# Kernel tuning notes

Hardware: AMD Instinct MI355X
Metric: run time of the kernel (lower is better)

Reference implementation:

```python
import jax, jax.numpy as jnp
import numpy as np

N = 100000   # nodes
E = 1600000  # edges
F = 13       # input features
H = 128      # hidden dim
G = 512      # graphs in batch
C = 10       # classes
EPS = 1e-5   # BatchNorm eps


def setup_inputs() -> dict:
    key = jax.random.key(0)
    ks = jax.random.split(key, 12)
    inp = {
        "x": jax.random.normal(ks[0], (N, F), dtype=jnp.float32),
        "edge_index": jax.random.randint(ks[1], (2, E), 0, N, dtype=jnp.int64),
        "batch": jnp.sort(jax.random.randint(ks[2], (N,), 0, G, dtype=jnp.int64)),
        "W1": jax.random.normal(ks[3], (F, H), dtype=jnp.float32) / np.sqrt(F),
        "b1": jnp.zeros((H,), jnp.float32),
        "g1": jnp.ones((H,), jnp.float32), "be1": jnp.zeros((H,), jnp.float32),
        "m1": jnp.zeros((H,), jnp.float32), "v1": jnp.ones((H,), jnp.float32),
        "W2": jax.random.normal(ks[4], (H, H), dtype=jnp.float32) / np.sqrt(H),
        "b2": jnp.zeros((H,), jnp.float32),
        "g2": jnp.ones((H,), jnp.float32), "be2": jnp.zeros((H,), jnp.float32),
        "m2": jnp.zeros((H,), jnp.float32), "v2": jnp.ones((H,), jnp.float32),
        "W3": jax.random.normal(ks[5], (H, H), dtype=jnp.float32) / np.sqrt(H),
        "b3": jnp.zeros((H,), jnp.float32),
        "g3": jnp.ones((H,), jnp.float32), "be3": jnp.zeros((H,), jnp.float32),
        "m3": jnp.zeros((H,), jnp.float32), "v3": jnp.ones((H,), jnp.float32),
        "Wc1": jax.random.normal(ks[6], (H, H // 2), dtype=jnp.float32) / np.sqrt(H),
        "bc1": jnp.zeros((H // 2,), jnp.float32),
        "Wc2": jax.random.normal(ks[7], (H // 2, C), dtype=jnp.float32) / np.sqrt(H // 2),
        "bc2": jnp.zeros((C,), jnp.float32),
    }
    return inp


def reference(x, edge_index, batch,
              W1, b1, g1, be1, m1, v1,
              W2, b2, g2, be2, m2, v2,
              W3, b3, g3, be3, m3, v3,
              Wc1, bc1, Wc2, bc2):
    src, dst = edge_index[0], edge_index[1]
    n = x.shape[0]
    # GCN symmetric norm with self-loops: deg = in-degree(A) + 1
    deg = jax.ops.segment_sum(jnp.ones(src.shape[0], x.dtype), dst, num_segments=n) + 1.0
    dis = jax.lax.rsqrt(deg)                    # D^{-1/2}
    enorm = dis[src] * dis[dst]                 # per-edge norm [E]
    snorm = dis * dis                           # self-loop norm [N]

    def gcn(h, W, b):
        h = h @ W                               # [N,H]
        msg = h[src] * enorm[:, None]           # gather + scale [E,H]
        agg = jax.ops.segment_sum(msg, dst, num_segments=n)  # scatter-add
        return agg + h * snorm[:, None] + b

    def bn(h, g, be, m, v):                     # eval-mode BatchNorm1d
        return (h - m) * jax.lax.rsqrt(v + EPS) * g + be

    h = jax.nn.relu(bn(gcn(x, W1, b1), g1, be1, m1, v1))
    h = jax.nn.relu(bn(gcn(h, W2, b2), g2, be2, m2, v2))
    h = jax.nn.relu(bn(gcn(h, W3, b3), g3, be3, m3, v3))
    # dropout is identity in eval mode

    # global mean pool over graphs
    sums = jax.ops.segment_sum(h, batch, num_segments=G)            # [G,H]
    cnts = jax.ops.segment_sum(jnp.ones(n, h.dtype), batch, num_segments=G)
    pooled = sums / jnp.maximum(cnts, 1.0)[:, None]

    hid = jax.nn.relu(pooled @ Wc1 + bc1)
    logits = hid @ Wc2 + bc2                                        # [G,C]
    return logits
```

## Files before the change

### kernel.cpp

```cpp
#include <hip/hip_runtime.h>
#include <hip/hip_bf16.h>

#define EPS 1e-5f

typedef unsigned short u16;
typedef unsigned int u32;
typedef __attribute__((ext_vector_type(8))) short bf16x8;
typedef __attribute__((ext_vector_type(4))) float f32x4;

__device__ __forceinline__ u32 f2bf(float f) {
  u32 u = __float_as_uint(f);
  return (u + 0x7FFFu + ((u >> 16) & 1u)) >> 16;
}
__device__ __forceinline__ u32 pack2bf(float lo, float hi) {
  return f2bf(lo) | (f2bf(hi) << 16);
}
__device__ __forceinline__ float4 bf4(uint2 u) {
  float4 r;
  r.x = __uint_as_float(u.x << 16);
  r.y = __uint_as_float(u.x & 0xFFFF0000u);
  r.z = __uint_as_float(u.y << 16);
  r.w = __uint_as_float(u.y & 0xFFFF0000u);
  return r;
}

__global__ void k_hist_rank(const int* __restrict__ dst, int* __restrict__ cnt,
                            int* __restrict__ rank, int E) {
  int i = blockIdx.x * blockDim.x + threadIdx.x;
  int i4 = i << 2;
  if (i4 + 3 < E) {
    int d0 = dst[i4], d1 = dst[i4 + 1], d2 = dst[i4 + 2], d3 = dst[i4 + 3];
    int r0 = atomicAdd(&cnt[d0], 1);
    int r1 = atomicAdd(&cnt[d1], 1);
    int r2 = atomicAdd(&cnt[d2], 1);
    int r3 = atomicAdd(&cnt[d3], 1);
    rank[i4] = r0; rank[i4 + 1] = r1; rank[i4 + 2] = r2; rank[i4 + 3] = r3;
  } else {
    for (int e = i4; e < E; ++e) rank[e] = atomicAdd(&cnt[dst[e]], 1);
  }
}

__global__ void k_dis(const int* __restrict__ cnt, float* __restrict__ dis, int N) {
  int i = blockIdx.x * blockDim.x + threadIdx.x;
  if (i < N) dis[i] = rsqrtf((float)cnt[i] + 1.0f);
}

__global__ void k_scan_block(const int* __restrict__ in, int* __restrict__ out,
                             int* __restrict__ bsum, int N) {
  __shared__ int tmp[256];
  int lid = threadIdx.x;
  int i = blockIdx.x * 256 + lid;
  int v = (i < N) ? in[i] : 0;
  tmp[lid] = v;
  __syncthreads();
  for (int off = 1; off < 256; off <<= 1) {
    int t = (lid >= off) ? tmp[lid - off] : 0;
    __syncthreads();
    tmp[lid] += t;
    __syncthreads();
  }
  if (i < N) out[i] = tmp[lid] - v;
  if (lid == 255) bsum[blockIdx.x] = tmp[255];
}

__global__ void k_scan_bsum(const int* __restrict__ bsum, int* __restrict__ bexc, int nb) {
  __shared__ int tmp[512];
  int lid = threadIdx.x;
  int v = (lid < nb) ? bsum[lid] : 0;
  tmp[lid] = v;
  __syncthreads();
  for (int off = 1; off < 512; off <<= 1) {
    int t = (lid >= off) ? tmp[lid - off] : 0;
    __syncthreads();
    tmp[lid] += t;
    __syncthreads();
  }
  if (lid < nb) bexc[lid] = tmp[lid] - v;
}

__global__ void k_add_back(int* __restrict__ offs, const int* __restrict__ bexc,
                           int N, int E) {
  int i = blockIdx.x * 256 + threadIdx.x;
  if (i < N) offs[i] += bexc[blockIdx.x];
  if (i == 0) offs[N] = E;
}

__global__ void k_fill_rank(const int* __restrict__ src, const int* __restrict__ dst,
                            const int* __restrict__ rank, const int* __restrict__ offs,
                            int* __restrict__ csr, int E) {
  int i = blockIdx.x * blockDim.x + threadIdx.x;
  int i4 = i << 2;
  if (i4 + 3 < E) {
    int s0 = src[i4], s1 = src[i4 + 1], s2 = src[i4 + 2], s3 = src[i4 + 3];
    int d0 = dst[i4], d1 = dst[i4 + 1], d2 = dst[i4 + 2], d3 = dst[i4 + 3];
    int r0 = rank[i4], r1 = rank[i4 + 1], r2 = rank[i4 + 2], r3 = rank[i4 + 3];
    int p0 = offs[d0] + r0;
    int p1 = offs[d1] + r1;
    int p2 = offs[d2] + r2;
    int p3 = offs[d3] + r3;
    csr[p0] = s0; csr[p1] = s1; csr[p2] = s2; csr[p3] = s3;
  } else {
    for (int e = i4; e < E; ++e) csr[offs[dst[e]] + rank[e]] = src[e];
  }
}

__global__ void k_prep_w(const float* __restrict__ W2, const float* __restrict__ W3,
                         const float* __restrict__ b2, const float* __restrict__ g2,
                         const float* __restrict__ be2, const float* __restrict__ m2,
                         const float* __restrict__ v2,
                         const float* __restrict__ b3, const float* __restrict__ g3,
                         const float* __restrict__ be3, const float* __restrict__ m3,
                         const float* __restrict__ v3,
                         u16* __restrict__ Wht2, u16* __restrict__ Wlt2,
                         u16* __restrict__ Wht3, u16* __restrict__ Wlt3,
                         float* __restrict__ sc2, float* __restrict__ tc2,
                         float* __restrict__ sc3, float* __restrict__ tc3) {
  int idx = blockIdx.x * 256 + threadIdx.x;
  int layer = idx >> 14;
  int e = idx & 16383;
  int c = e >> 7, k = e & 127;
  const float* W = layer ? W3 : W2;
  float w = W[k * 128 + c];
  u32 h = f2bf(w);
  float l = w - __uint_as_float(h << 16);
  u16* Wh = layer ? Wht3 : Wht2;
  u16* Wl = layer ? Wlt3 : Wlt2;
  Wh[e] = (u16)h;
  Wl[e] = (u16)f2bf(l);
  if (e < 128) {
    int ch = e;
    const float* gg = layer ? g3 : g2;  const float* vv = layer ? v3 : v2;
    const float* be = layer ? be3 : be2; const float* mm = layer ? m3 : m2;
    const float* bb = layer ? b3 : b2;
    float s = gg[ch] * rsqrtf(vv[ch] + EPS);
    (layer ? sc3 : sc2)[ch] = s;
    (layer ? tc3 : tc2)[ch] = be[ch] + (bb[ch] - mm[ch]) * s;
  }
}

__global__ void k_padx_scale(const float* __restrict__ x, const float* __restrict__ dis,
                             float* __restrict__ xs, int N) {
  int i = blockIdx.x * blockDim.x + threadIdx.x;
  if (i >= N * 16) return;
  int n = i >> 4, f = i & 15;
  xs[i] = (f < 13) ? x[n * 13 + f] * dis[n] : 0.0f;
}

__global__ __launch_bounds__(64) void k_agg16(
    const float* __restrict__ xs, const int* __restrict__ csr,
    const int* __restrict__ offs, const float* __restrict__ dis,
    float* __restrict__ out, int N) {
  int node = (blockIdx.x << 2) + (threadIdx.x >> 4);
  int f = threadIdx.x & 15;
  if (node >= N) return;
  float a0 = xs[(size_t)node * 16 + f];
  float a1 = 0.f, a2 = 0.f, a3 = 0.f;
  int beg = offs[node], end = offs[node + 1];
  int i = beg;
  for (; i + 4 <= end; i += 4) {
    int s0 = csr[i], s1 = csr[i + 1], s2 = csr[i + 2], s3 = csr[i + 3];
    a0 += xs[(size_t)s0 * 16 + f];
    a1 += xs[(size_t)s1 * 16 + f];
    a2 += xs[(size_t)s2 * 16 + f];
    a3 += xs[(size_t)s3 * 16 + f];
  }
  for (; i < end; ++i) a0 += xs[(size_t)csr[i] * 16 + f];
  out[(size_t)node * 16 + f] = dis[node] * ((a0 + a1) + (a2 + a3));
}

__global__ __launch_bounds__(256) void k_gemm1(
    const float* __restrict__ ax, const float* __restrict__ W1,
    const float* __restrict__ bb, const float* __restrict__ gg,
    const float* __restrict__ be, const float* __restrict__ mm,
    const float* __restrict__ vv, const float* __restrict__ dis,
    u32* __restrict__ outb, int N) {
  int idx = blockIdx.x * 256 + threadIdx.x;
  if (idx >= N * 64) return;
  int node = idx >> 6, cp = idx & 63;
  int c0 = cp * 2, c1 = c0 + 1;
  float s0 = gg[c0] * rsqrtf(vv[c0] + EPS);
  float t0 = be[c0] + (bb[c0] - mm[c0]) * s0;
  float s1 = gg[c1] * rsqrtf(vv[c1] + EPS);
  float t1 = be[c1] + (bb[c1] - mm[c1]) * s1;
  float acc0 = 0.f, acc1 = 0.f;
#pragma unroll
  for (int k = 0; k < 13; ++k) {
    float av = ax[(size_t)node * 16 + k];
    acc0 = fmaf(av, W1[k * 128 + c0], acc0);
    acc1 = fmaf(av, W1[k * 128 + c1], acc1);
  }
  float dn = dis[node];
  float o0 = dn * fmaxf(fmaf(acc0, s0, t0), 0.f);
  float o1 = dn * fmaxf(fmaf(acc1, s1, t1), 0.f);
  outb[(size_t)node * 64 + cp] = pack2bf(o0, o1);
}

__global__ __launch_bounds__(256) void k_agg128(
    const u16* __restrict__ hb, const int* __restrict__ csr,
    const int* __restrict__ offs, const float* __restrict__ dis,
    uint2* __restrict__ Ahp, uint2* __restrict__ Alp, int N) {
  int node = (blockIdx.x << 2) + (threadIdx.x >> 6);
  if (node >= N) return;
  const int lane = threadIdx.x & 63;
  const int half = lane >> 5;
  const int q = lane & 31;
  const uint2* __restrict__ h2p = (const uint2*)hb;
  float dn = dis[node];
  int beg = offs[node], end = offs[node + 1];

  float4 sv = bf4(h2p[(size_t)node * 32 + q]);
  float wsf = half ? 0.f : 1.f;
  float4 a0 = make_float4(sv.x * wsf, sv.y * wsf, sv.z * wsf, sv.w * wsf);
  float4 z = make_float4(0.f, 0.f, 0.f, 0.f);
  float4 a1 = z, a2 = z, a3 = z, a4 = z, a5 = z, a6 = z, a7 = z;

  int i = beg;
  for (; i + 16 <= end; i += 16) {
    int s0 = csr[i +  0 + half];
    int s1 = csr[i +  2 + half];
    int s2 = csr[i +  4 + half];
    int s3 = csr[i +  6 + half];
    int s4 = csr[i +  8 + half];
    int s5 = csr[i + 10 + half];
    int s6 = csr[i + 12 + half];
    int s7 = csr[i + 14 + half];
    uint2 u0 = h2p[(size_t)s0 * 32 + q];
    uint2 u1 = h2p[(size_t)s1 * 32 + q];
    uint2 u2 = h2p[(size_t)s2 * 32 + q];
    uint2 u3 = h2p[(size_t)s3 * 32 + q];
    uint2 u4 = h2p[(size_t)s4 * 32 + q];
    uint2 u5 = h2p[(size_t)s5 * 32 + q];
    uint2 u6 = h2p[(size_t)s6 * 32 + q];
    uint2 u7 = h2p[(size_t)s7 * 32 + q];
    float4 v0 = bf4(u0), v1 = bf4(u1), v2 = bf4(u2), v3 = bf4(u3);
    float4 v4 = bf4(u4), v5 = bf4(u5), v6 = bf4(u6), v7 = bf4(u7);
    a0.x += v0.x; a0.y += v0.y; a0.z += v0.z; a0.w += v0.w;
    a1.x += v1.x; a1.y += v1.y; a1.z += v1.z; a1.w += v1.w;
    a2.x += v2.x; a2.y += v2.y; a2.z += v2.z; a2.w += v2.w;
    a3.x += v3.x; a3.y += v3.y; a3.z += v3.z; a3.w += v3.w;
    a4.x += v4.x; a4.y += v4.y; a4.z += v4.z; a4.w += v4.w;
    a5.x += v5.x; a5.y += v5.y; a5.z += v5.z; a5.w += v5.w;
    a6.x += v6.x; a6.y += v6.y; a6.z += v6.z; a6.w += v6.w;
    a7.x += v7.x; a7.y += v7.y; a7.z += v7.z; a7.w += v7.w;
  }
  for (; i < end; i += 2) {
    int j = i + half;
    int jc = (j < end) ? j : (end - 1);
    int s = csr[jc];
    float wt = (j < end) ? 1.f : 0.f;
    float4 v = bf4(h2p[(size_t)s * 32 + q]);
    a0.x = fmaf(v.x, wt, a0.x); a0.y = fmaf(v.y, wt, a0.y);
    a0.z = fmaf(v.z, wt, a0.z); a0.w = fmaf(v.w, wt, a0.w);
  }

  float4 r;
  r.x = ((a0.x + a1.x) + (a2.x + a3.x)) + ((a4.x + a5.x) + (a6.x + a7.x));
  r.y = ((a0.y + a1.y) + (a2.y + a3.y)) + ((a4.y + a5.y) + (a6.y + a7.y));
  r.z = ((a0.z + a1.z) + (a2.z + a3.z)) + ((a4.z + a5.z) + (a6.z + a7.z));
  r.w = ((a0.w + a1.w) + (a2.w + a3.w)) + ((a4.w + a5.w) + (a6.w + a7.w));
  r.x += __shfl_xor(r.x, 32, 64);
  r.y += __shfl_xor(r.y, 32, 64);
  r.z += __shfl_xor(r.z, 32, 64);
  r.w += __shfl_xor(r.w, 32, 64);
  if (half == 0) {
    r.x *= dn; r.y *= dn; r.z *= dn; r.w *= dn;
    u32 hx = f2bf(r.x), hy = f2bf(r.y), hz = f2bf(r.z), hw = f2bf(r.w);
    uint2 ph = make_uint2(hx | (hy << 16), hz | (hw << 16));
    float lx = r.x - __uint_as_float(hx << 16);
    float ly = r.y - __uint_as_float(hy << 16);
    float lz = r.z - __uint_as_float(hz << 16);
    float lw = r.w - __uint_as_float(hw << 16);
    uint2 pl = make_uint2(pack2bf(lx, ly), pack2bf(lz, lw));
    Ahp[(size_t)node * 32 + q] = ph;
    Alp[(size_t)node * 32 + q] = pl;
  }
}

template <bool OB>
__global__ __launch_bounds__(256) void k_gemm_mfma(
    const u16* __restrict__ Ah, const u16* __restrict__ Al,
    const u16* __restrict__ Wht, const u16* __restrict__ Wlt,
    const float* __restrict__ sc, const float* __restrict__ tc,
    const float* __restrict__ dis,
    float* __restrict__ outf, u16* __restrict__ outb, int N) {
  const int lane = threadIdx.x & 63;
  const int wv = threadIdx.x >> 6;
  const int r0 = blockIdx.x * 128 + wv * 32;
  const int lr = lane & 15;
  const int kg = lane >> 4;

  bf16x8 ahf[2][4], alf[2][4];
#pragma unroll
  for (int rt = 0; rt < 2; ++rt) {
    int row = min(r0 + rt * 16 + lr, N - 1);
    const bf16x8* pAh = (const bf16x8*)(Ah + (size_t)row * 128 + kg * 8);
    const bf16x8* pAl = (const bf16x8*)(Al + (size_t)row * 128 + kg * 8);
#pragma unroll
    for (int ks = 0; ks < 4; ++ks) {
      ahf[rt][ks] = pAh[ks * 4];
      alf[rt][ks] = pAl[ks * 4];
    }
  }
  float dr[2][4];
  if (OB) {
#pragma unroll
    for (int rt = 0; rt < 2; ++rt)
#pragma unroll
      for (int j = 0; j < 4; ++j)
        dr[rt][j] = dis[min(r0 + rt * 16 + kg * 4 + j, N - 1)];
  }

#pragma unroll
  for (int ct = 0; ct < 8; ++ct) {
    int c = ct * 16 + lr;
    const bf16x8* pBh = (const bf16x8*)(Wht + (size_t)c * 128 + kg * 8);
    const bf16x8* pBl = (const bf16x8*)(Wlt + (size_t)c * 128 + kg * 8);
    bf16x8 bh[4], bl[4];
#pragma unroll
    for (int ks = 0; ks < 4; ++ks) { bh[ks] = pBh[ks * 4]; bl[ks] = pBl[ks * 4]; }
    float s = sc[c], t = tc[c];
#pragma unroll
    for (int rt = 0; rt < 2; ++rt) {
      f32x4 acc = {0.f, 0.f, 0.f, 0.f};
#pragma unroll
      for (int ks = 0; ks < 4; ++ks) {
        acc = __builtin_amdgcn_mfma_f32_16x16x32_bf16(ahf[rt][ks], bh[ks], acc, 0, 0, 0);
        acc = __builtin_amdgcn_mfma_f32_16x16x32_bf16(alf[rt][ks], bh[ks], acc, 0, 0, 0);
        acc = __builtin_amdgcn_mfma_f32_16x16x32_bf16(ahf[rt][ks], bl[ks], acc, 0, 0, 0);
      }
#pragma unroll
      for (int j = 0; j < 4; ++j) {
        int row = r0 + rt * 16 + kg * 4 + j;
        if (row < N) {
          float o = fmaxf(fmaf(acc[j], s, t), 0.f);
          if (OB) {
            outb[(size_t)row * 128 + c] = (u16)f2bf(o * dr[rt][j]);
          } else {
            outf[(size_t)row * 128 + c] = o;
          }
        }
      }
    }
  }
}

__global__ void k_cnt_batch(const int* __restrict__ batch, int* __restrict__ cnt,
                            int N, int G) {
  int g = blockIdx.x * blockDim.x + threadIdx.x;
  if (g >= G) return;
  int lo = 0, hi = N;
  while (lo < hi) { int m = (lo + hi) >> 1; if (batch[m] < g) lo = m + 1; else hi = m; }
  int lb = lo;
  lo = 0; hi = N;
  while (lo < hi) { int m = (lo + hi) >> 1; if (batch[m] <= g) lo = m + 1; else hi = m; }
  cnt[g] = lo - lb;
}

__global__ __launch_bounds__(128) void k_pool(
    const float* __restrict__ h, const int* __restrict__ batch,
    float* __restrict__ pooled, int N) {
  int f = threadIdx.x;
  int n0 = blockIdx.x * 128;
  int nEnd = min(n0 + 128, N);
  float acc = 0.f;
  int cur = -1;
  for (int nn = n0; nn < nEnd; ++nn) {
    int g = batch[nn];
    if (g != cur) {
      if (cur >= 0) atomicAdd(&pooled[cur * 128 + f], acc);
      cur = g;
      acc = 0.f;
    }
    acc += h[(size_t)nn * 128 + f];
  }
  if (cur >= 0) atomicAdd(&pooled[cur * 128 + f], acc);
}

__global__ __launch_bounds__(64) void k_cls(
    const float* __restrict__ pooled, const int* __restrict__ cnt,
    const float* __restrict__ Wc1, const float* __restrict__ bc1,
    const float* __restrict__ Wc2, const float* __restrict__ bc2,
    float* __restrict__ out, int G) {
  __shared__ float pm[128];
  __shared__ float hid[64];
  int g = blockIdx.x, t = threadIdx.x;
  float invc = 1.f / fmaxf((float)cnt[g], 1.f);
  pm[t]      = pooled[g * 128 + t] * invc;
  pm[t + 64] = pooled[g * 128 + 64 + t] * invc;
  __syncthreads();
  float a = bc1[t];
#pragma unroll 8
  for (int k = 0; k < 128; ++k) a = fmaf(pm[k], Wc1[k * 64 + t], a);
  hid[t] = fmaxf(a, 0.f);
  __syncthreads();
  if (t < 10) {
    float a2 = bc2[t];
#pragma unroll
    for (int j = 0; j < 64; ++j) a2 = fmaf(hid[j], Wc2[j * 10 + t], a2);
    out[g * 10 + t] = a2;
  }
}

extern "C" void kernel_launch(void* const* d_in, const int* in_sizes, int n_in,
                              void* d_out, int out_size, void* d_ws, size_t ws_size,
                              hipStream_t stream) {
  const float* x   = (const float*)d_in[0];
  const int*   ei  = (const int*)d_in[1];
  const int* batch = (const int*)d_in[2];
  const float* W1 = (const float*)d_in[3];
  const float* b1 = (const float*)d_in[4];
  const float* g1 = (const float*)d_in[5];
  const float* be1 = (const float*)d_in[6];
  const float* m1 = (const float*)d_in[7];
  const float* v1 = (const float*)d_in[8];
  const float* W2 = (const float*)d_in[9];
  const float* b2 = (const float*)d_in[10];
  const float* g2 = (const float*)d_in[11];
  const float* be2 = (const float*)d_in[12];
  const float* m2 = (const float*)d_in[13];
  const float* v2 = (const float*)d_in[14];
  const float* W3 = (const float*)d_in[15];
  const float* b3 = (const float*)d_in[16];
  const float* g3 = (const float*)d_in[17];
  const float* be3 = (const float*)d_in[18];
  const float* m3 = (const float*)d_in[19];
  const float* v3 = (const float*)d_in[20];
  const float* Wc1 = (const float*)d_in[21];
  const float* bc1 = (const float*)d_in[22];
  const float* Wc2 = (const float*)d_in[23];
  const float* bc2 = (const float*)d_in[24];

  const int N = in_sizes[0] / 13;
  const int E = in_sizes[1] / 2;
  const int G = out_size / 10;
  const int* src = ei;
  const int* dst = ei + E;

  char* ws = (char*)d_ws;
  size_t off = 0;
  auto alloc = [&](size_t bytes) {
    char* p = ws + off;
    off = (off + bytes + 255) & ~(size_t)255;
    return p;
  };
  int*   deg    = (int*)  alloc((size_t)N * 4);
  float* dis    = (float*)alloc((size_t)N * 4);
  int*   offs   = (int*)  alloc((size_t)(N + 1) * 4);
  const int nb  = (N + 255) / 256;
  int*   bsum   = (int*)  alloc((size_t)nb * 4);
  int*   bexc   = (int*)  alloc((size_t)nb * 4);
  int*   rank   = (int*)  alloc((size_t)E * 4);
  int*   csr    = (int*)  alloc((size_t)E * 4);
  u16*   hbf    = (u16*)  alloc((size_t)N * 128 * 2);
  u16*   Ahp    = (u16*)  alloc((size_t)N * 128 * 2);
  u16*   Alp    = (u16*)  alloc((size_t)N * 128 * 2);
  float* bufF   = (float*)alloc((size_t)N * 128 * 4);
  u16*   Wht2   = (u16*)  alloc(16384 * 2);
  u16*   Wlt2   = (u16*)  alloc(16384 * 2);
  u16*   Wht3   = (u16*)  alloc(16384 * 2);
  u16*   Wlt3   = (u16*)  alloc(16384 * 2);
  float* sc2    = (float*)alloc(128 * 4);
  float* tc2    = (float*)alloc(128 * 4);
  float* sc3    = (float*)alloc(128 * 4);
  float* tc3    = (float*)alloc(128 * 4);
  float* pooled = (float*)alloc((size_t)G * 128 * 4);
  int*   cntg   = (int*)  alloc((size_t)G * 4);
  float* xs = bufF;
  float* ax = (float*)Ahp;

  hipMemsetAsync(deg, 0, (size_t)N * 4, stream);
  hipMemsetAsync(pooled, 0, (size_t)G * 128 * 4, stream);

  k_prep_w<<<128, 256, 0, stream>>>(W2, W3, b2, g2, be2, m2, v2, b3, g3, be3, m3, v3,
                                    Wht2, Wlt2, Wht3, Wlt3, sc2, tc2, sc3, tc3);

  const int nE4 = (E + 3) / 4;
  k_hist_rank<<<(nE4 + 255) / 256, 256, 0, stream>>>(dst, deg, rank, E);
  k_dis<<<(N + 255) / 256, 256, 0, stream>>>(deg, dis, N);
  k_scan_block<<<nb, 256, 0, stream>>>(deg, offs, bsum, N);
  k_scan_bsum<<<1, 512, 0, stream>>>(bsum, bexc, nb);
  k_add_back<<<nb, 256, 0, stream>>>(offs, bexc, N, E);
  k_fill_rank<<<(nE4 + 255) / 256, 256, 0, stream>>>(src, dst, rank, offs, csr, E);

  k_padx_scale<<<(N * 16 + 255) / 256, 256, 0, stream>>>(x, dis, xs, N);
  k_agg16<<<(N + 3) / 4, 64, 0, stream>>>(xs, csr, offs, dis, ax, N);
  k_gemm1<<<(N * 64 + 255) / 256, 256, 0, stream>>>(ax, W1, b1, g1, be1, m1, v1, dis,
                                                    (u32*)hbf, N);

  const int gemmGrid = (N + 127) / 128;
  k_agg128<<<(N + 3) / 4, 256, 0, stream>>>(hbf, csr, offs, dis,
                                            (uint2*)Ahp, (uint2*)Alp, N);
  k_gemm_mfma<true><<<gemmGrid, 256, 0, stream>>>(Ahp, Alp, Wht2, Wlt2, sc2, tc2, dis,
                                                  nullptr, hbf, N);
  k_agg128<<<(N + 3) / 4, 256, 0, stream>>>(hbf, csr, offs, dis,
                                            (uint2*)Ahp, (uint2*)Alp, N);
  k_gemm_mfma<false><<<gemmGrid, 256, 0, stream>>>(Ahp, Alp, Wht3, Wlt3, sc3, tc3, dis,
                                                   bufF, nullptr, N);

  k_cnt_batch<<<(G + 255) / 256, 256, 0, stream>>>(batch, cntg, N, G);
  k_pool<<<(N + 127) / 128, 128, 0, stream>>>(bufF, batch, pooled, N);
  k_cls<<<G, 64, 0, stream>>>(pooled, cntg, Wc1, bc1, Wc2, bc2, (float*)d_out, G);
}
```

Before: 640.4 us.

## Pad CSR rows to multiples of four with a zero dummy node, widen agg loads

```diff
diff --git a/kernel.cpp b/kernel.cpp
--- a/kernel.cpp
+++ b/kernel.cpp
@@ -15,13 +15,10 @@
 __device__ __forceinline__ u32 pack2bf(float lo, float hi) {
   return f2bf(lo) | (f2bf(hi) << 16);
 }
-__device__ __forceinline__ float4 bf4(uint2 u) {
-  float4 r;
-  r.x = __uint_as_float(u.x << 16);
-  r.y = __uint_as_float(u.x & 0xFFFF0000u);
-  r.z = __uint_as_float(u.y << 16);
-  r.w = __uint_as_float(u.y & 0xFFFF0000u);
-  return r;
+
+__device__ __forceinline__ void dacc(float2& a, u32 u) {
+  a.x += __uint_as_float(u << 16);
+  a.y += __uint_as_float(u & 0xFFFF0000u);
 }
 
 __global__ void k_hist_rank(const int* __restrict__ dst, int* __restrict__ cnt,
@@ -40,9 +37,14 @@
   }
 }
 
-__global__ void k_dis(const int* __restrict__ cnt, float* __restrict__ dis, int N) {
+__global__ void k_dis_pdeg(const int* __restrict__ cnt, float* __restrict__ dis,
+                           int* __restrict__ pdeg, int N) {
   int i = blockIdx.x * blockDim.x + threadIdx.x;
-  if (i < N) dis[i] = rsqrtf((float)cnt[i] + 1.0f);
+  if (i < N) {
+    int d = cnt[i];
+    dis[i] = rsqrtf((float)d + 1.0f);
+    pdeg[i] = (d + 3) & ~3;
+  }
 }
 
 __global__ void k_scan_block(const int* __restrict__ in, int* __restrict__ out,
@@ -79,10 +81,10 @@
 }
 
 __global__ void k_add_back(int* __restrict__ offs, const int* __restrict__ bexc,
-                           int N, int E) {
+                           const int* __restrict__ bsum, int N, int nb) {
   int i = blockIdx.x * 256 + threadIdx.x;
   if (i < N) offs[i] += bexc[blockIdx.x];
-  if (i == 0) offs[N] = E;
+  if (i == 0) offs[N] = bexc[nb - 1] + bsum[nb - 1];
 }
 
 __global__ void k_fill_rank(const int* __restrict__ src, const int* __restrict__ dst,
@@ -94,14 +96,21 @@
     int s0 = src[i4], s1 = src[i4 + 1], s2 = src[i4 + 2], s3 = src[i4 + 3];
     int d0 = dst[i4], d1 = dst[i4 + 1], d2 = dst[i4 + 2], d3 = dst[i4 + 3];
     int r0 = rank[i4], r1 = rank[i4 + 1], r2 = rank[i4 + 2], r3 = rank[i4 + 3];
-    int p0 = offs[d0] + r0;
-    int p1 = offs[d1] + r1;
-    int p2 = offs[d2] + r2;
-    int p3 = offs[d3] + r3;
-    csr[p0] = s0; csr[p1] = s1; csr[p2] = s2; csr[p3] = s3;
+    csr[offs[d0] + r0] = s0;
+    csr[offs[d1] + r1] = s1;
+    csr[offs[d2] + r2] = s2;
+    csr[offs[d3] + r3] = s3;
   } else {
     for (int e = i4; e < E; ++e) csr[offs[dst[e]] + rank[e]] = src[e];
   }
+}
+
+__global__ void k_pad_fill(const int* __restrict__ deg, const int* __restrict__ offs,
+                           int* __restrict__ csr, int N) {
+  int n = blockIdx.x * blockDim.x + threadIdx.x;
+  if (n >= N) return;
+  int b = offs[n] + deg[n], e = offs[n + 1];
+  for (int j = b; j < e; ++j) csr[j] = N;
 }
 
 __global__ void k_prep_w(const float* __restrict__ W2, const float* __restrict__ W3,
@@ -141,9 +150,9 @@
 __global__ void k_padx_scale(const float* __restrict__ x, const float* __restrict__ dis,
                              float* __restrict__ xs, int N) {
   int i = blockIdx.x * blockDim.x + threadIdx.x;
-  if (i >= N * 16) return;
+  if (i >= (N + 1) * 16) return;
   int n = i >> 4, f = i & 15;
-  xs[i] = (f < 13) ? x[n * 13 + f] * dis[n] : 0.0f;
+  xs[i] = (n < N && f < 13) ? x[n * 13 + f] * dis[n] : 0.0f;
 }
 
 __global__ __launch_bounds__(64) void k_agg16(
@@ -151,20 +160,18 @@
     const int* __restrict__ offs, const float* __restrict__ dis,
     float* __restrict__ out, int N) {
   int node = (blockIdx.x << 2) + (threadIdx.x >> 4);
+  if (node >= N) return;
   int f = threadIdx.x & 15;
-  if (node >= N) return;
   float a0 = xs[(size_t)node * 16 + f];
   float a1 = 0.f, a2 = 0.f, a3 = 0.f;
   int beg = offs[node], end = offs[node + 1];
-  int i = beg;
-  for (; i + 4 <= end; i += 4) {
-    int s0 = csr[i], s1 = csr[i + 1], s2 = csr[i + 2], s3 = csr[i + 3];
-    a0 += xs[(size_t)s0 * 16 + f];
-    a1 += xs[(size_t)s1 * 16 + f];
-    a2 += xs[(size_t)s2 * 16 + f];
-    a3 += xs[(size_t)s3 * 16 + f];
-  }
-  for (; i < end; ++i) a0 += xs[(size_t)csr[i] * 16 + f];
+  for (int i = beg; i < end; i += 4) {
+    int4 s4 = *(const int4*)(csr + i);
+    a0 += xs[(size_t)s4.x * 16 + f];
+    a1 += xs[(size_t)s4.y * 16 + f];
+    a2 += xs[(size_t)s4.z * 16 + f];
+    a3 += xs[(size_t)s4.w * 16 + f];
+  }
   out[(size_t)node * 16 + f] = dis[node] * ((a0 + a1) + (a2 + a3));
 }
 
@@ -175,8 +182,9 @@
     const float* __restrict__ vv, const float* __restrict__ dis,
     u32* __restrict__ outb, int N) {
   int idx = blockIdx.x * 256 + threadIdx.x;
-  if (idx >= N * 64) return;
+  if (idx >= (N + 1) * 64) return;
   int node = idx >> 6, cp = idx & 63;
+  if (node == N) { outb[(size_t)node * 64 + cp] = 0u; return; }
   int c0 = cp * 2, c1 = c0 + 1;
   float s0 = gg[c0] * rsqrtf(vv[c0] + EPS);
   float t0 = be[c0] + (bb[c0] - mm[c0]) * s0;
@@ -198,81 +206,72 @@
 __global__ __launch_bounds__(256) void k_agg128(
     const u16* __restrict__ hb, const int* __restrict__ csr,
     const int* __restrict__ offs, const float* __restrict__ dis,
-    uint2* __restrict__ Ahp, uint2* __restrict__ Alp, int N) {
+    uint4* __restrict__ Ahp, uint4* __restrict__ Alp, int N) {
   int node = (blockIdx.x << 2) + (threadIdx.x >> 6);
   if (node >= N) return;
+  node = __builtin_amdgcn_readfirstlane(node);
   const int lane = threadIdx.x & 63;
-  const int half = lane >> 5;
-  const int q = lane & 31;
-  const uint2* __restrict__ h2p = (const uint2*)hb;
-  float dn = dis[node];
+  const int qt = lane >> 4;
+  const int q = lane & 15;
+  const uint4* __restrict__ H = (const uint4*)hb;
   int beg = offs[node], end = offs[node + 1];
 
-  float4 sv = bf4(h2p[(size_t)node * 32 + q]);
-  float wsf = half ? 0.f : 1.f;
-  float4 a0 = make_float4(sv.x * wsf, sv.y * wsf, sv.z * wsf, sv.w * wsf);
-  float4 z = make_float4(0.f, 0.f, 0.f, 0.f);
-  float4 a1 = z, a2 = z, a3 = z, a4 = z, a5 = z, a6 = z, a7 = z;
+  float2 z2 = make_float2(0.f, 0.f);
+  float2 aA0 = z2, aA1 = z2, aA2 = z2, aA3 = z2;
+  float2 aB0 = z2, aB1 = z2, aB2 = z2, aB3 = z2;
+
+  {
+    uint4 su = H[(size_t)node * 16 + q];
+    if (qt == 0) { dacc(aA0, su.x); dacc(aA1, su.y); dacc(aA2, su.z); dacc(aA3, su.w); }
+  }
 
   int i = beg;
-  for (; i + 16 <= end; i += 16) {
-    int s0 = csr[i +  0 + half];
-    int s1 = csr[i +  2 + half];
-    int s2 = csr[i +  4 + half];
-    int s3 = csr[i +  6 + half];
-    int s4 = csr[i +  8 + half];
-    int s5 = csr[i + 10 + half];
-    int s6 = csr[i + 12 + half];
-    int s7 = csr[i + 14 + half];
-    uint2 u0 = h2p[(size_t)s0 * 32 + q];
-    uint2 u1 = h2p[(size_t)s1 * 32 + q];
-    uint2 u2 = h2p[(size_t)s2 * 32 + q];
-    uint2 u3 = h2p[(size_t)s3 * 32 + q];
-    uint2 u4 = h2p[(size_t)s4 * 32 + q];
-    uint2 u5 = h2p[(size_t)s5 * 32 + q];
-    uint2 u6 = h2p[(size_t)s6 * 32 + q];
-    uint2 u7 = h2p[(size_t)s7 * 32 + q];
-    float4 v0 = bf4(u0), v1 = bf4(u1), v2 = bf4(u2), v3 = bf4(u3);
-    float4 v4 = bf4(u4), v5 = bf4(u5), v6 = bf4(u6), v7 = bf4(u7);
-    a0.x += v0.x; a0.y += v0.y; a0.z += v0.z; a0.w += v0.w;
-    a1.x += v1.x; a1.y += v1.y; a1.z += v1.z; a1.w += v1.w;
-    a2.x += v2.x; a2.y += v2.y; a2.z += v2.z; a2.w += v2.w;
-    a3.x += v3.x; a3.y += v3.y; a3.z += v3.z; a3.w += v3.w;
-    a4.x += v4.x; a4.y += v4.y; a4.z += v4.z; a4.w += v4.w;
-    a5.x += v5.x; a5.y += v5.y; a5.z += v5.z; a5.w += v5.w;
-    a6.x += v6.x; a6.y += v6.y; a6.z += v6.z; a6.w += v6.w;
-    a7.x += v7.x; a7.y += v7.y; a7.z += v7.z; a7.w += v7.w;
-  }
-  for (; i < end; i += 2) {
-    int j = i + half;
-    int jc = (j < end) ? j : (end - 1);
-    int s = csr[jc];
-    float wt = (j < end) ? 1.f : 0.f;
-    float4 v = bf4(h2p[(size_t)s * 32 + q]);
-    a0.x = fmaf(v.x, wt, a0.x); a0.y = fmaf(v.y, wt, a0.y);
-    a0.z = fmaf(v.z, wt, a0.z); a0.w = fmaf(v.w, wt, a0.w);
-  }
-
-  float4 r;
-  r.x = ((a0.x + a1.x) + (a2.x + a3.x)) + ((a4.x + a5.x) + (a6.x + a7.x));
-  r.y = ((a0.y + a1.y) + (a2.y + a3.y)) + ((a4.y + a5.y) + (a6.y + a7.y));
-  r.z = ((a0.z + a1.z) + (a2.z + a3.z)) + ((a4.z + a5.z) + (a6.z + a7.z));
-  r.w = ((a0.w + a1.w) + (a2.w + a3.w)) + ((a4.w + a5.w) + (a6.w + a7.w));
-  r.x += __shfl_xor(r.x, 32, 64);
-  r.y += __shfl_xor(r.y, 32, 64);
-  r.z += __shfl_xor(r.z, 32, 64);
-  r.w += __shfl_xor(r.w, 32, 64);
-  if (half == 0) {
-    r.x *= dn; r.y *= dn; r.z *= dn; r.w *= dn;
-    u32 hx = f2bf(r.x), hy = f2bf(r.y), hz = f2bf(r.z), hw = f2bf(r.w);
-    uint2 ph = make_uint2(hx | (hy << 16), hz | (hw << 16));
-    float lx = r.x - __uint_as_float(hx << 16);
-    float ly = r.y - __uint_as_float(hy << 16);
-    float lz = r.z - __uint_as_float(hz << 16);
-    float lw = r.w - __uint_as_float(hw << 16);
-    uint2 pl = make_uint2(pack2bf(lx, ly), pack2bf(lz, lw));
-    Ahp[(size_t)node * 32 + q] = ph;
-    Alp[(size_t)node * 32 + q] = pl;
+  for (; i + 8 <= end; i += 8) {
+    int4 sA = *(const int4*)(csr + i);
+    int4 sB = *(const int4*)(csr + i + 4);
+    int ea = (qt == 0) ? sA.x : (qt == 1) ? sA.y : (qt == 2) ? sA.z : sA.w;
+    int eb = (qt == 0) ? sB.x : (qt == 1) ? sB.y : (qt == 2) ? sB.z : sB.w;
+    uint4 uA = H[(size_t)ea * 16 + q];
+    uint4 uB = H[(size_t)eb * 16 + q];
+    dacc(aA0, uA.x); dacc(aA1, uA.y); dacc(aA2, uA.z); dacc(aA3, uA.w);
+    dacc(aB0, uB.x); dacc(aB1, uB.y); dacc(aB2, uB.z); dacc(aB3, uB.w);
+  }
+  if (i < end) {
+    int4 sA = *(const int4*)(csr + i);
+    int ea = (qt == 0) ? sA.x : (qt == 1) ? sA.y : (qt == 2) ? sA.z : sA.w;
+    uint4 uA = H[(size_t)ea * 16 + q];
+    dacc(aA0, uA.x); dacc(aA1, uA.y); dacc(aA2, uA.z); dacc(aA3, uA.w);
+  }
+
+  float r[8];
+  r[0] = aA0.x + aB0.x; r[1] = aA0.y + aB0.y;
+  r[2] = aA1.x + aB1.x; r[3] = aA1.y + aB1.y;
+  r[4] = aA2.x + aB2.x; r[5] = aA2.y + aB2.y;
+  r[6] = aA3.x + aB3.x; r[7] = aA3.y + aB3.y;
+#pragma unroll
+  for (int j = 0; j < 8; ++j) {
+    r[j] += __shfl_xor(r[j], 16, 64);
+    r[j] += __shfl_xor(r[j], 32, 64);
+  }
+  if (qt == 0) {
+    float dn = dis[node];
+    uint4 ph, pl;
+    u32 hw[8];
+#pragma unroll
+    for (int j = 0; j < 8; ++j) { r[j] *= dn; hw[j] = f2bf(r[j]); }
+    ph.x = hw[0] | (hw[1] << 16);
+    ph.y = hw[2] | (hw[3] << 16);
+    ph.z = hw[4] | (hw[5] << 16);
+    ph.w = hw[6] | (hw[7] << 16);
+    float l[8];
+#pragma unroll
+    for (int j = 0; j < 8; ++j) l[j] = r[j] - __uint_as_float(hw[j] << 16);
+    pl.x = pack2bf(l[0], l[1]);
+    pl.y = pack2bf(l[2], l[3]);
+    pl.z = pack2bf(l[4], l[5]);
+    pl.w = pack2bf(l[6], l[7]);
+    Ahp[(size_t)node * 16 + q] = ph;
+    Alp[(size_t)node * 16 + q] = pl;
   }
 }
 
@@ -445,16 +444,17 @@
   };
   int*   deg    = (int*)  alloc((size_t)N * 4);
   float* dis    = (float*)alloc((size_t)N * 4);
+  int*   pdeg   = (int*)  alloc((size_t)N * 4);
   int*   offs   = (int*)  alloc((size_t)(N + 1) * 4);
   const int nb  = (N + 255) / 256;
   int*   bsum   = (int*)  alloc((size_t)nb * 4);
   int*   bexc   = (int*)  alloc((size_t)nb * 4);
   int*   rank   = (int*)  alloc((size_t)E * 4);
-  int*   csr    = (int*)  alloc((size_t)E * 4);
-  u16*   hbf    = (u16*)  alloc((size_t)N * 128 * 2);
+  int*   csr    = (int*)  alloc(((size_t)E + 3 * (size_t)N + 8) * 4);
+  u16*   hbf    = (u16*)  alloc((size_t)(N + 1) * 128 * 2);
   u16*   Ahp    = (u16*)  alloc((size_t)N * 128 * 2);
   u16*   Alp    = (u16*)  alloc((size_t)N * 128 * 2);
-  float* bufF   = (float*)alloc((size_t)N * 128 * 4);
+  float* bufF   = (float*)alloc((size_t)(N + 1) * 128 * 4);
   u16*   Wht2   = (u16*)  alloc(16384 * 2);
   u16*   Wlt2   = (u16*)  alloc(16384 * 2);
   u16*   Wht3   = (u16*)  alloc(16384 * 2);
@@ -476,24 +476,25 @@
 
   const int nE4 = (E + 3) / 4;
   k_hist_rank<<<(nE4 + 255) / 256, 256, 0, stream>>>(dst, deg, rank, E);
-  k_dis<<<(N + 255) / 256, 256, 0, stream>>>(deg, dis, N);
-  k_scan_block<<<nb, 256, 0, stream>>>(deg, offs, bsum, N);
+  k_dis_pdeg<<<(N + 255) / 256, 256, 0, stream>>>(deg, dis, pdeg, N);
+  k_scan_block<<<nb, 256, 0, stream>>>(pdeg, offs, bsum, N);
   k_scan_bsum<<<1, 512, 0, stream>>>(bsum, bexc, nb);
-  k_add_back<<<nb, 256, 0, stream>>>(offs, bexc, N, E);
+  k_add_back<<<nb, 256, 0, stream>>>(offs, bexc, bsum, N, nb);
   k_fill_rank<<<(nE4 + 255) / 256, 256, 0, stream>>>(src, dst, rank, offs, csr, E);
-
-  k_padx_scale<<<(N * 16 + 255) / 256, 256, 0, stream>>>(x, dis, xs, N);
+  k_pad_fill<<<(N + 255) / 256, 256, 0, stream>>>(deg, offs, csr, N);
+
+  k_padx_scale<<<((N + 1) * 16 + 255) / 256, 256, 0, stream>>>(x, dis, xs, N);
   k_agg16<<<(N + 3) / 4, 64, 0, stream>>>(xs, csr, offs, dis, ax, N);
-  k_gemm1<<<(N * 64 + 255) / 256, 256, 0, stream>>>(ax, W1, b1, g1, be1, m1, v1, dis,
-                                                    (u32*)hbf, N);
+  k_gemm1<<<((N + 1) * 64 + 255) / 256, 256, 0, stream>>>(ax, W1, b1, g1, be1, m1, v1,
+                                                          dis, (u32*)hbf, N);
 
   const int gemmGrid = (N + 127) / 128;
   k_agg128<<<(N + 3) / 4, 256, 0, stream>>>(hbf, csr, offs, dis,
-                                            (uint2*)Ahp, (uint2*)Alp, N);
+                                            (uint4*)Ahp, (uint4*)Alp, N);
   k_gemm_mfma<true><<<gemmGrid, 256, 0, stream>>>(Ahp, Alp, Wht2, Wlt2, sc2, tc2, dis,
                                                   nullptr, hbf, N);
   k_agg128<<<(N + 3) / 4, 256, 0, stream>>>(hbf, csr, offs, dis,
-                                            (uint2*)Ahp, (uint2*)Alp, N);
+                                            (uint4*)Ahp, (uint4*)Alp, N);
   k_gemm_mfma<false><<<gemmGrid, 256, 0, stream>>>(Ahp, Alp, Wht3, Wlt3, sc3, tc3, dis,
                                                    bufF, nullptr, N);
 
```

Result: faster. 586.9 us (-8.4%).
